# Kernel optimization log

Hardware: AMD Instinct MI355X
Metric: run time of the kernel (lower is better)

Reference implementation:

```python
import jax, jax.numpy as jnp
import numpy as np

H = 256  # rnn hidden size

def _rnn_dir(x, wih, whh, bih, bhh):
    # x: [B,T,D] -> outputs [B,T,H]; h_t = tanh(x_t Wih^T + bih + h_{t-1} Whh^T + bhh)
    xproj = jnp.einsum('btd,hd->bth', x, wih) + bih + bhh  # precompute input projection
    def step(h, xp):
        h = jnp.tanh(xp + h @ whh.T)
        return h, h
    h0 = jnp.zeros((x.shape[0], whh.shape[0]), x.dtype)
    _, ys = jax.lax.scan(step, h0, jnp.swapaxes(xproj, 0, 1))
    return jnp.swapaxes(ys, 0, 1)

def _birnn(x, wif, whf, bif, bhf, wib, whb, bib, bhb):
    fwd = _rnn_dir(x, wif, whf, bif, bhf)
    bwd = _rnn_dir(x[:, ::-1, :], wib, whb, bib, bhb)[:, ::-1, :]
    return jnp.concatenate([fwd, bwd], axis=-1)

def setup_inputs() -> dict:
    key = jax.random.key(0)
    ks = jax.random.split(key, 24)
    B, T, V, E = 64, 512, 131072, 128
    s = 0.05
    emb = jax.random.normal(ks[0], (V, E), jnp.float32) * s
    emb = emb.at[0].set(0.0)  # padding_idx=0
    def W(k, shp):
        return jax.random.normal(k, shp, jnp.float32) * s
    inp = {
        'x': jax.random.randint(ks[1], (B, T), 0, V),
        'emb': emb,
        'r1_wif': W(ks[2], (H, E)), 'r1_whf': W(ks[3], (H, H)),
        'r1_bif': W(ks[4], (H,)), 'r1_bhf': W(ks[5], (H,)),
        'r1_wib': W(ks[6], (H, E)), 'r1_whb': W(ks[7], (H, H)),
        'r1_bib': W(ks[8], (H,)), 'r1_bhb': W(ks[9], (H,)),
        'r2_wif': W(ks[10], (H, 2 * H)), 'r2_whf': W(ks[11], (H, H)),
        'r2_bif': W(ks[12], (H,)), 'r2_bhf': W(ks[13], (H,)),
        'r2_wib': W(ks[14], (H, 2 * H)), 'r2_whb': W(ks[15], (H, H)),
        'r2_bib': W(ks[16], (H,)), 'r2_bhb': W(ks[17], (H,)),
        'ln_g': jnp.ones((1024,), jnp.float32),
        'ln_b': jnp.zeros((1024,), jnp.float32),
        'w1': W(ks[18], (512, 1024)), 'b1': W(ks[19], (512,)),
        'w2': W(ks[20], (256, 512)), 'b2': W(ks[21], (256,)),
    }
    return inp

def reference(x, emb, r1_wif, r1_whf, r1_bif, r1_bhf, r1_wib, r1_whb, r1_bib, r1_bhb,
              r2_wif, r2_whf, r2_bif, r2_bhf, r2_wib, r2_whb, r2_bib, r2_bhb,
              ln_g, ln_b, w1, b1, w2, b2):
    e = emb[x]  # [B,T,128]
    o1 = _birnn(e, r1_wif, r1_whf, r1_bif, r1_bhf, r1_wib, r1_whb, r1_bib, r1_bhb)  # [B,T,512]
    o2 = _birnn(o1, r2_wif, r2_whf, r2_bif, r2_bhf, r2_wib, r2_whb, r2_bib, r2_bhb)  # [B,T,512]
    last = o2[:, -1, :]
    mean = jnp.mean(o2, axis=1)
    h = jnp.concatenate([last, mean], axis=1)  # [B,1024]
    mu = jnp.mean(h, axis=-1, keepdims=True)
    var = jnp.mean(jnp.square(h - mu), axis=-1, keepdims=True)
    h = (h - mu) * jax.lax.rsqrt(var + 1e-5) * ln_g + ln_b
    h = jax.nn.relu(h @ w1.T + b1)
    return h @ w2.T + b2
```

## Files before the change

kernel.cpp:

```cpp
#include <hip/hip_runtime.h>
#include <stdint.h>

typedef unsigned short u16;
typedef unsigned int   u32;
typedef __attribute__((ext_vector_type(8))) short short8;
typedef __attribute__((ext_vector_type(4))) float f32x4;

#define T_LEN 512
#define HID   256
#define C2LE 2.8853900817779268f

__device__ __forceinline__ float bflo(u32 u){ union{u32 i; float f;} v; v.i = u << 16; return v.f; }
__device__ __forceinline__ float bfhi(u32 u){ union{u32 i; float f;} v; v.i = u & 0xffff0000u; return v.f; }
__device__ __forceinline__ float b2f(u16 s){ union{u32 i; float f;} v; v.i = ((u32)s) << 16; return v.f; }
__device__ __forceinline__ u16 f2b(float f){
  union{float f; u32 i;} v; v.f = f;
  u32 r = v.i + 0x7fffu + ((v.i >> 16) & 1u);
  return (u16)(r >> 16);
}
__device__ __forceinline__ u32 pk2(float a, float b){ return (u32)f2b(a) | ((u32)f2b(b) << 16); }
__device__ __forceinline__ u32 cvtpk(float a, float b){
  u32 r; asm("v_cvt_pk_bf16_f32 %0, %1, %2" : "=v"(r) : "v"(a), "v"(b)); return r;
}
__device__ __forceinline__ float tanh_pre(float y){
#if __has_builtin(__builtin_amdgcn_exp2f)
  float e = __builtin_amdgcn_exp2f(y);
#else
  float e = exp2f(y);
#endif
  return __builtin_fmaf(-2.f, __builtin_amdgcn_rcpf(e + 1.f), 1.f);
}
__device__ __forceinline__ bool flag_bf16(const u32* f){ return (f[0] & 0xFFFFu) == 0x3F80u; }

#define NT 22
struct ConvArgs {
  const void* src[NT];
  u32 off[NT];
  u32 total;
  const u32* flagsrc;
};

__global__ __launch_bounds__(256)
void convert_params(ConvArgs a, u16* __restrict__ dst)
{
  const bool bf = flag_bf16(a.flagsrc);
  const u32 stride = gridDim.x * blockDim.x;
  for (u32 g = blockIdx.x * blockDim.x + threadIdx.x; g < a.total; g += stride) {
    int t = 0;
    #pragma unroll
    for (int i = 1; i < NT; ++i) t += (g >= a.off[i]);
    u32 local = g - a.off[t];
    float v = bf ? b2f(((const u16*)a.src[t])[local])
                 : ((const float*)a.src[t])[local];
    if (t == 1 || t == 5 || t == 9 || t == 13) v *= C2LE;
    dst[g] = f2b(v);
  }
}

template<int K, int SRC>
__global__ __launch_bounds__(256, 2)
void wgemm(const void* Bsrc, const int* __restrict__ gidx,
           const u16* __restrict__ Wf, const u16* __restrict__ Wb,
           const u16* __restrict__ bif, const u16* __restrict__ bhf,
           const u16* __restrict__ bib, const u16* __restrict__ bhb,
           u16* outT, const u32* flagsrc)
{
  __shared__ __align__(16) u16 lds[64 * K];
  const int tid  = threadIdx.x;
  const int row0 = blockIdx.x * 64;
  const int bb   = row0 >> 9;
  const int t0   = row0 & 511;
  const int bt   = bb >> 4, nb = bb & 15;
  constexpr int CPR = K / 8;

  bool abf = true;
  if (SRC == 0) abf = flag_bf16(flagsrc);

  for (int i = tid; i < 64 * CPR; i += 256) {
    int r = i / CPR, c = i % CPR;
    uint4 v;
    if (SRC == 0) {
      long rb = (long)gidx[row0 + r] * K;
      if (abf) {
        v = *(const uint4*)((const u16*)Bsrc + rb + c * 8);
      } else {
        const float* af = (const float*)Bsrc;
        float4 lo = *(const float4*)(af + rb + c * 8);
        float4 hi = *(const float4*)(af + rb + c * 8 + 4);
        v.x = pk2(lo.x, lo.y); v.y = pk2(lo.z, lo.w);
        v.z = pk2(hi.x, hi.y); v.w = pk2(hi.z, hi.w);
      }
    } else {
      int k = c * 8, d = k >> 8;
      size_t e = (size_t)(d * 4 + bt) * 2097152 + (size_t)(t0 + r) * 4096
               + (size_t)nb * 256 + (k & 255);
      v = *(const uint4*)((const u16*)Bsrc + e);
    }
    *(uint4*)&lds[r * K + ((c ^ (r & 7)) * 8)] = v;
  }
  __syncthreads();

  const int w = tid >> 6, lane = tid & 63, n16 = lane & 15, quad = lane >> 4;
  const int d = w >> 1;
  const u16* W  = d ? Wb : Wf;
  const u16* bi = d ? bib : bif;
  const u16* bh = d ? bhb : bhf;
  const int mbase = (w & 1) * 128;

  f32x4 acc[8][4];
  #pragma unroll
  for (int i = 0; i < 8; ++i)
    #pragma unroll
    for (int j = 0; j < 4; ++j) acc[i][j] = (f32x4){0.f, 0.f, 0.f, 0.f};

  #pragma unroll
  for (int kk = 0; kk < K / 32; ++kk) {
    short8 bfr[4];
    #pragma unroll
    for (int j = 0; j < 4; ++j) {
      int r = j * 16 + n16;
      int c = (kk * 4 + quad) ^ (r & 7);
      bfr[j] = *(const short8*)&lds[r * K + c * 8];
    }
    #pragma unroll
    for (int i = 0; i < 8; ++i) {
      short8 afr = *(const short8*)(W + (size_t)(mbase + i * 16 + n16) * K + kk * 32 + quad * 8);
      #pragma unroll
      for (int j = 0; j < 4; ++j)
        acc[i][j] = __builtin_amdgcn_mfma_f32_16x16x32_bf16(afr, bfr[j], acc[i][j], 0, 0, 0);
    }
  }

  #pragma unroll
  for (int i = 0; i < 8; ++i) {
    int mrow0 = mbase + i * 16 + quad * 4;
    uint2 biv = *(const uint2*)(bi + mrow0);
    uint2 bhv = *(const uint2*)(bh + mrow0);
    float bias0 = b2f(biv.x & 0xffff) + b2f(bhv.x & 0xffff);
    float bias1 = b2f(biv.x >> 16)    + b2f(bhv.x >> 16);
    float bias2 = b2f(biv.y & 0xffff) + b2f(bhv.y & 0xffff);
    float bias3 = b2f(biv.y >> 16)    + b2f(bhv.y >> 16);
    #pragma unroll
    for (int j = 0; j < 4; ++j) {
      int t = t0 + j * 16 + n16;
      uint2 pv;
      pv.x = cvtpk(C2LE * (acc[i][j][0] + bias0), C2LE * (acc[i][j][1] + bias1));
      pv.y = cvtpk(C2LE * (acc[i][j][2] + bias2), C2LE * (acc[i][j][3] + bias3));
      size_t e = (size_t)(d * 4 + bt) * 2097152 + (size_t)t * 4096
               + (size_t)nb * 256 + mrow0;
      *(uint2*)(outT + e) = pv;
    }
  }
}

template<int MODE>
__device__ __forceinline__ void scan_step5(
    int s, int send,
    const u16* hrp,
    u16* hwp,
    uint2& pf,
    const u16*& xptr, u16*& optr, int pstep,
    const short8 (&wa)[8], f32x4& sum, float* lastb, int lbase)
{
  short8 hb[8];
  #pragma unroll
  for (int kk = 0; kk < 8; ++kk)
    hb[kk] = *(const short8*)(hrp + kk * 32);

  uint2 xv = pf;
  pf = *(const uint2*)(xptr);
  xptr += pstep;

  f32x4 a = (f32x4){bflo(xv.x), bfhi(xv.x), bflo(xv.y), bfhi(xv.y)};
  f32x4 b = (f32x4){0.f, 0.f, 0.f, 0.f};
  #pragma unroll
  for (int kk = 0; kk < 8; kk += 2) {
    a = __builtin_amdgcn_mfma_f32_16x16x32_bf16(wa[kk],     hb[kk],     a, 0, 0, 0);
    b = __builtin_amdgcn_mfma_f32_16x16x32_bf16(wa[kk + 1], hb[kk + 1], b, 0, 0, 0);
  }

  float h0 = tanh_pre(a[0] + b[0]);
  float h1 = tanh_pre(a[1] + b[1]);
  float h2 = tanh_pre(a[2] + b[2]);
  float h3 = tanh_pre(a[3] + b[3]);
  uint2 hv; hv.x = cvtpk(h0, h1); hv.y = cvtpk(h2, h3);
  *(uint2*)(hwp) = hv;

  if (MODE == 0) {
    *(uint2*)(optr) = hv;
    optr += pstep;
  } else {
    sum += (f32x4){h0, h1, h2, h3};
    if (s == send)
      *(float4*)&lastb[lbase] = (float4){h0, h1, h2, h3};
  }

  asm volatile("s_waitcnt lgkmcnt(0)" ::: "memory");
  __builtin_amdgcn_s_barrier();
  asm volatile("" ::: "memory");
}

template<int MODE>
__global__ __launch_bounds__(1024, 4)
void rnn_scan(const u16* xpT,
              const u16* __restrict__ whhF, const u16* __restrict__ whhB,
              u16* o1T, float* __restrict__ lastb, float* __restrict__ sumb)
{
  __shared__ __align__(16) u16 hl[2][16][264];
  const int tid = threadIdx.x, w = tid >> 6, lane = tid & 63;
  const int n16 = lane & 15, quad = lane >> 4;
  const int dir = blockIdx.x >> 2, bt = blockIdx.x & 3;
  const u16* whh = dir ? whhB : whhF;
  const int m0 = w * 16 + quad * 4;

  short8 wa[8];
  #pragma unroll
  for (int kk = 0; kk < 8; ++kk)
    wa[kk] = *(const short8*)(whh + (size_t)(w * 16 + n16) * 256 + kk * 32 + quad * 8);

  for (int i = tid; i < 16 * 264; i += 1024) ((u16*)hl[0])[i] = 0;

  const size_t blkbase = (size_t)(dir * 4 + bt) * 2097152;
  const int t0    = dir ? 511 : 0;
  const int pstep = dir ? -4096 : 4096;
  const u16* xptr = xpT + blkbase + (size_t)t0 * 4096 + n16 * 256 + m0;
  u16*       optr = o1T + blkbase + (size_t)t0 * 4096 + n16 * 256 + m0;
  const int lbase = (dir * 64 + bt * 16 + n16) * 256 + m0;
  const int send  = dir ? 0 : 511;

  const u16* hr0 = &hl[0][n16][quad * 8];
  const u16* hr1 = &hl[1][n16][quad * 8];
  u16* hw0 = &hl[1][n16][m0];
  u16* hw1 = &hl[0][n16][m0];

  uint2 pf0, pf1;
  pf0 = *(const uint2*)(xptr); xptr += pstep;
  pf1 = *(const uint2*)(xptr); xptr += pstep;

  f32x4 sum = (f32x4){0.f, 0.f, 0.f, 0.f};
  __syncthreads();

  for (int s = 0; s < 512; s += 2) {
    scan_step5<MODE>(s,     send, hr0, hw0, pf0, xptr, optr, pstep, wa, sum, lastb, lbase);
    scan_step5<MODE>(s + 1, send, hr1, hw1, pf1, xptr, optr, pstep, wa, sum, lastb, lbase);
  }

  if (MODE == 1)
    *(float4*)&sumb[lbase] = (float4){sum[0], sum[1], sum[2], sum[3]};
}

__device__ __forceinline__ float dot8(uint4 q, const float* hp){
  return bflo(q.x)*hp[0] + bfhi(q.x)*hp[1] + bflo(q.y)*hp[2] + bfhi(q.y)*hp[3]
       + bflo(q.z)*hp[4] + bfhi(q.z)*hp[5] + bflo(q.w)*hp[6] + bfhi(q.w)*hp[7];
}

__global__ __launch_bounds__(256)
void head_kernel(const float* __restrict__ lastb, const float* __restrict__ sumb,
                 const u16* __restrict__ g, const u16* __restrict__ be,
                 const u16* __restrict__ w1, const u16* __restrict__ b1,
                 const u16* __restrict__ w2, const u16* __restrict__ b2,
                 void* outv, const u32* flagsrc)
{
  __shared__ __align__(16) float hv[1024];
  __shared__ __align__(16) float act[512];
  __shared__ float red[8];
  const int tid = threadIdx.x;
  const int b   = blockIdx.x;
  const bool bf = flag_bf16(flagsrc);

  float v0 = lastb[b * 256 + tid];
  float v1 = lastb[(64 + b) * 256 + tid];
  float v2 = sumb[b * 256 + tid] * (1.f / 512.f);
  float v3 = sumb[(64 + b) * 256 + tid] * (1.f / 512.f);
  hv[tid] = v0; hv[256 + tid] = v1; hv[512 + tid] = v2; hv[768 + tid] = v3;

  float s  = v0 + v1 + v2 + v3;
  float ss = v0*v0 + v1*v1 + v2*v2 + v3*v3;
  #pragma unroll
  for (int off = 32; off; off >>= 1) {
    s  += __shfl_down(s, off);
    ss += __shfl_down(ss, off);
  }
  if ((tid & 63) == 0) { red[tid >> 6] = s; red[4 + (tid >> 6)] = ss; }
  __syncthreads();
  float S  = red[0] + red[1] + red[2] + red[3];
  float SS = red[4] + red[5] + red[6] + red[7];
  float mu   = S * (1.f / 1024.f);
  float var  = SS * (1.f / 1024.f) - mu * mu;
  float rstd = rsqrtf(var + 1e-5f);

  #pragma unroll
  for (int i = 0; i < 4; ++i) {
    int idx = i * 256 + tid;
    hv[idx] = (hv[idx] - mu) * rstd * b2f(g[idx]) + b2f(be[idx]);
  }
  __syncthreads();

  #pragma unroll
  for (int jj = 0; jj < 2; ++jj) {
    int j = jj * 256 + tid;
    const uint4* wr = (const uint4*)(w1 + (long)j * 1024);
    float a = 0.f;
    for (int c = 0; c < 128; ++c) a += dot8(wr[c], &hv[c * 8]);
    a += b2f(b1[j]);
    act[j] = a > 0.f ? a : 0.f;
  }
  __syncthreads();

  const uint4* wr2 = (const uint4*)(w2 + (long)tid * 512);
  float a = 0.f;
  for (int c = 0; c < 64; ++c) a += dot8(wr2[c], &act[c * 8]);
  a += b2f(b2[tid]);

  if (bf) {
    ((u16*)outv)[b * 256 + tid] = f2b(a);
  } else {
    union { u32 i; float f; } u; u.i = ((u32)f2b(a)) << 16;
    ((float*)outv)[b * 256 + tid] = u.f;
  }
}

extern "C" void kernel_launch(void* const* d_in, const int* in_sizes, int n_in,
                              void* d_out, int out_size, void* d_ws, size_t ws_size,
                              hipStream_t stream)
{
  const int* x    = (const int*)d_in[0];
  const u32* flag = (const u32*)d_in[18];

  static const int sizes[NT] = {
    32768, 65536, 256, 256, 32768, 65536, 256, 256,
    131072, 65536, 256, 256, 131072, 65536, 256, 256,
    1024, 1024, 524288, 512, 131072, 256
  };
  ConvArgs ca;
  u32 off = 0;
  for (int i = 0; i < NT; ++i) {
    ca.src[i] = d_in[2 + i];
    ca.off[i] = off;
    off += (u32)sizes[i];
  }
  ca.total = off;
  ca.flagsrc = flag;

  char* ws = (char*)d_ws;
  u16*   buf    = (u16*)ws;
  u16*   pm     = (u16*)(ws + 33554432);
  float* lastb  = (float*)(ws + 36054528);
  float* sumb   = (float*)(ws + 36185600);

  const u16* p_r1wif = pm + 0;
  const u16* p_r1whf = pm + 32768;
  const u16* p_r1bif = pm + 98304;
  const u16* p_r1bhf = pm + 98560;
  const u16* p_r1wib = pm + 98816;
  const u16* p_r1whb = pm + 131584;
  const u16* p_r1bib = pm + 197120;
  const u16* p_r1bhb = pm + 197376;
  const u16* p_r2wif = pm + 197632;
  const u16* p_r2whf = pm + 328704;
  const u16* p_r2bif = pm + 394240;
  const u16* p_r2bhf = pm + 394496;
  const u16* p_r2wib = pm + 394752;
  const u16* p_r2whb = pm + 525824;
  const u16* p_r2bib = pm + 591360;
  const u16* p_r2bhb = pm + 591616;
  const u16* p_lng   = pm + 591872;
  const u16* p_lnb   = pm + 592896;
  const u16* p_w1    = pm + 593920;
  const u16* p_b1    = pm + 1118208;
  const u16* p_w2    = pm + 1118720;
  const u16* p_b2    = pm + 1249792;

  convert_params<<<1024, 256, 0, stream>>>(ca, pm);

  wgemm<128, 0><<<512, 256, 0, stream>>>(d_in[1], x,
      p_r1wif, p_r1wib, p_r1bif, p_r1bhf, p_r1bib, p_r1bhb, buf, flag);
  rnn_scan<0><<<8, 1024, 0, stream>>>(buf, p_r1whf, p_r1whb, buf, nullptr, nullptr);
  wgemm<512, 1><<<512, 256, 0, stream>>>(buf, nullptr,
      p_r2wif, p_r2wib, p_r2bif, p_r2bhf, p_r2bib, p_r2bhb, buf, flag);
  rnn_scan<1><<<8, 1024, 0, stream>>>(buf, p_r2whf, p_r2whb, nullptr, lastb, sumb);
  head_kernel<<<64, 256, 0, stream>>>(lastb, sumb, p_lng, p_lnb, p_w1, p_b1, p_w2, p_b2,
      d_out, flag);
}
```

Before: 948.6 us.

## Use 512-thread layer-2 scan with two 16-row output tiles per wave

Adds a new layer-2 RNN scan kernel that runs 8 waves per block instead of 16. Each wave computes two 16-row tiles of the hidden update, so the shared h fragments are reused across two weight tiles and fewer waves join each per-step barrier. The cost is twice the weight registers per wave and a longer MFMA chain per wave on every serial step. Layer 1 keeps the original 1024-thread scan.

```diff
diff --git a/kernel.cpp b/kernel.cpp
--- a/kernel.cpp
+++ b/kernel.cpp
@@ -156,9 +156,7 @@
 template<int MODE>
 __device__ __forceinline__ void scan_step5(
     int s, int send,
-    const u16* hrp,
-    u16* hwp,
-    uint2& pf,
+    const u16* hrp, u16* hwp, uint2& pf,
     const u16*& xptr, u16*& optr, int pstep,
     const short8 (&wa)[8], f32x4& sum, float* lastb, int lbase)
 {
@@ -247,6 +245,112 @@
 
   if (MODE == 1)
     *(float4*)&sumb[lbase] = (float4){sum[0], sum[1], sum[2], sum[3]};
+}
+
+__device__ __forceinline__ void scan_step8(
+    int s, int send,
+    const u16* hrp, u16* hwp, uint2 (&pf)[2],
+    const u16*& xptr, int pstep,
+    const short8 (&wa)[2][8], f32x4 (&sum)[2], float* lastb, int lbase)
+{
+  short8 hb[8];
+  #pragma unroll
+  for (int kk = 0; kk < 8; ++kk)
+    hb[kk] = *(const short8*)(hrp + kk * 32);
+
+  uint2 xv0 = pf[0], xv1 = pf[1];
+  pf[0] = *(const uint2*)(xptr);
+  pf[1] = *(const uint2*)(xptr + 16);
+  xptr += pstep;
+
+  f32x4 a0 = (f32x4){bflo(xv0.x), bfhi(xv0.x), bflo(xv0.y), bfhi(xv0.y)};
+  f32x4 a1 = (f32x4){bflo(xv1.x), bfhi(xv1.x), bflo(xv1.y), bfhi(xv1.y)};
+  f32x4 b0 = (f32x4){0.f, 0.f, 0.f, 0.f};
+  f32x4 b1 = (f32x4){0.f, 0.f, 0.f, 0.f};
+  #pragma unroll
+  for (int kk = 0; kk < 8; kk += 2) {
+    a0 = __builtin_amdgcn_mfma_f32_16x16x32_bf16(wa[0][kk],     hb[kk],     a0, 0, 0, 0);
+    a1 = __builtin_amdgcn_mfma_f32_16x16x32_bf16(wa[1][kk],     hb[kk],     a1, 0, 0, 0);
+    b0 = __builtin_amdgcn_mfma_f32_16x16x32_bf16(wa[0][kk + 1], hb[kk + 1], b0, 0, 0, 0);
+    b1 = __builtin_amdgcn_mfma_f32_16x16x32_bf16(wa[1][kk + 1], hb[kk + 1], b1, 0, 0, 0);
+  }
+
+  float h00 = tanh_pre(a0[0] + b0[0]), h01 = tanh_pre(a0[1] + b0[1]);
+  float h02 = tanh_pre(a0[2] + b0[2]), h03 = tanh_pre(a0[3] + b0[3]);
+  float h10 = tanh_pre(a1[0] + b1[0]), h11 = tanh_pre(a1[1] + b1[1]);
+  float h12 = tanh_pre(a1[2] + b1[2]), h13 = tanh_pre(a1[3] + b1[3]);
+
+  uint2 hv0; hv0.x = cvtpk(h00, h01); hv0.y = cvtpk(h02, h03);
+  uint2 hv1; hv1.x = cvtpk(h10, h11); hv1.y = cvtpk(h12, h13);
+  *(uint2*)(hwp)      = hv0;
+  *(uint2*)(hwp + 16) = hv1;
+
+  sum[0] += (f32x4){h00, h01, h02, h03};
+  sum[1] += (f32x4){h10, h11, h12, h13};
+  if (s == send) {
+    *(float4*)&lastb[lbase]      = (float4){h00, h01, h02, h03};
+    *(float4*)&lastb[lbase + 16] = (float4){h10, h11, h12, h13};
+  }
+
+  asm volatile("s_waitcnt lgkmcnt(0)" ::: "memory");
+  __builtin_amdgcn_s_barrier();
+  asm volatile("" ::: "memory");
+}
+
+__global__ __launch_bounds__(512, 2)
+void rnn_scan8(const u16* xpT,
+               const u16* __restrict__ whhF, const u16* __restrict__ whhB,
+               float* __restrict__ lastb, float* __restrict__ sumb)
+{
+  __shared__ __align__(16) u16 hl[2][16][264];
+  const int tid = threadIdx.x, w = tid >> 6, lane = tid & 63;
+  const int n16 = lane & 15, quad = lane >> 4;
+  const int dir = blockIdx.x >> 2, bt = blockIdx.x & 3;
+  const u16* whh = dir ? whhB : whhF;
+
+  short8 wa[2][8];
+  #pragma unroll
+  for (int j = 0; j < 2; ++j)
+    #pragma unroll
+    for (int kk = 0; kk < 8; ++kk)
+      wa[j][kk] = *(const short8*)(whh + (size_t)(w * 32 + j * 16 + n16) * 256
+                                       + kk * 32 + quad * 8);
+
+  for (int i = tid; i < 16 * 264; i += 512) ((u16*)hl[0])[i] = 0;
+
+  const size_t blkbase = (size_t)(dir * 4 + bt) * 2097152;
+  const int t0    = dir ? 511 : 0;
+  const int pstep = dir ? -4096 : 4096;
+  const int m0    = w * 32 + quad * 4;
+  const u16* xptr = xpT + blkbase + (size_t)t0 * 4096 + n16 * 256 + m0;
+  const int lbase = (dir * 64 + bt * 16 + n16) * 256 + m0;
+  const int send  = dir ? 0 : 511;
+
+  const u16* hr0 = &hl[0][n16][quad * 8];
+  const u16* hr1 = &hl[1][n16][quad * 8];
+  u16* hw0 = &hl[1][n16][m0];
+  u16* hw1 = &hl[0][n16][m0];
+
+  uint2 pf0[2], pf1[2];
+  pf0[0] = *(const uint2*)(xptr);
+  pf0[1] = *(const uint2*)(xptr + 16);
+  xptr += pstep;
+  pf1[0] = *(const uint2*)(xptr);
+  pf1[1] = *(const uint2*)(xptr + 16);
+  xptr += pstep;
+
+  f32x4 sum[2];
+  sum[0] = (f32x4){0.f, 0.f, 0.f, 0.f};
+  sum[1] = (f32x4){0.f, 0.f, 0.f, 0.f};
+  __syncthreads();
+
+  for (int s = 0; s < 512; s += 2) {
+    scan_step8(s,     send, hr0, hw0, pf0, xptr, pstep, wa, sum, lastb, lbase);
+    scan_step8(s + 1, send, hr1, hw1, pf1, xptr, pstep, wa, sum, lastb, lbase);
+  }
+
+  *(float4*)&sumb[lbase]      = (float4){sum[0][0], sum[0][1], sum[0][2], sum[0][3]};
+  *(float4*)&sumb[lbase + 16] = (float4){sum[1][0], sum[1][1], sum[1][2], sum[1][3]};
 }
 
 __device__ __forceinline__ float dot8(uint4 q, const float* hp){
@@ -378,7 +482,7 @@
   rnn_scan<0><<<8, 1024, 0, stream>>>(buf, p_r1whf, p_r1whb, buf, nullptr, nullptr);
   wgemm<512, 1><<<512, 256, 0, stream>>>(buf, nullptr,
       p_r2wif, p_r2wib, p_r2bif, p_r2bhf, p_r2bib, p_r2bhb, buf, flag);
-  rnn_scan<1><<<8, 1024, 0, stream>>>(buf, p_r2whf, p_r2whb, nullptr, lastb, sumb);
+  rnn_scan8<<<8, 512, 0, stream>>>(buf, p_r2whf, p_r2whb, lastb, sumb);
   head_kernel<<<64, 256, 0, stream>>>(lastb, sumb, p_lng, p_lnb, p_w1, p_b1, p_w2, p_b2,
       d_out, flag);
 }
```

Result: faster. 929.8 us (-2.0%).

## Split RNN scan batch rows across more workgroups with redundant MFMA columns

Applied to the files above, without the earlier changes.

The recurrent scan kernels now give each workgroup a subset of NB batch rows (8 for layer 1, 4 for layer 2) instead of 16, launching 16 or 32 workgroups instead of 8. The MFMA tile is still 16 columns wide, so lanes beyond NB compute duplicate columns and have their stores masked off. This spreads the serial per-timestep work over more compute units, cutting per-block latency and LDS pressure, at the cost of wasted MFMA throughput and repeated weight loads per block.

```diff
diff --git a/kernel.cpp b/kernel.cpp
--- a/kernel.cpp
+++ b/kernel.cpp
@@ -154,11 +154,9 @@
 }
 
 template<int MODE>
-__device__ __forceinline__ void scan_step5(
-    int s, int send,
-    const u16* hrp,
-    u16* hwp,
-    uint2& pf,
+__device__ __forceinline__ void scan_step6(
+    int s, int send, bool st,
+    const u16* hrp, u16* hwp, uint2& pf,
     const u16*& xptr, u16*& optr, int pstep,
     const short8 (&wa)[8], f32x4& sum, float* lastb, int lbase)
 {
@@ -184,14 +182,14 @@
   float h2 = tanh_pre(a[2] + b[2]);
   float h3 = tanh_pre(a[3] + b[3]);
   uint2 hv; hv.x = cvtpk(h0, h1); hv.y = cvtpk(h2, h3);
-  *(uint2*)(hwp) = hv;
+  if (st) *(uint2*)(hwp) = hv;
 
   if (MODE == 0) {
-    *(uint2*)(optr) = hv;
+    if (st) *(uint2*)(optr) = hv;
     optr += pstep;
   } else {
     sum += (f32x4){h0, h1, h2, h3};
-    if (s == send)
+    if (s == send && st)
       *(float4*)&lastb[lbase] = (float4){h0, h1, h2, h3};
   }
 
@@ -200,38 +198,45 @@
   asm volatile("" ::: "memory");
 }
 
-template<int MODE>
+template<int MODE, int NB>
 __global__ __launch_bounds__(1024, 4)
 void rnn_scan(const u16* xpT,
               const u16* __restrict__ whhF, const u16* __restrict__ whhB,
               u16* o1T, float* __restrict__ lastb, float* __restrict__ sumb)
 {
-  __shared__ __align__(16) u16 hl[2][16][264];
+  __shared__ __align__(16) u16 hl[2][NB][264];
   const int tid = threadIdx.x, w = tid >> 6, lane = tid & 63;
   const int n16 = lane & 15, quad = lane >> 4;
-  const int dir = blockIdx.x >> 2, bt = blockIdx.x & 3;
-  const u16* whh = dir ? whhB : whhF;
-  const int m0 = w * 16 + quad * 4;
+  constexpr int NSUB = 16 / NB;
+  constexpr int NBLK = 4 * NSUB;
+  const int dir   = blockIdx.x / NBLK;
+  const int rbl   = blockIdx.x % NBLK;
+  const int bt    = rbl / NSUB;
+  const int nbase = (rbl % NSUB) * NB;
+  const int rb    = n16 & (NB - 1);
+  const bool st   = (n16 < NB);
+  const u16* whh  = dir ? whhB : whhF;
+  const int m0    = w * 16 + quad * 4;
 
   short8 wa[8];
   #pragma unroll
   for (int kk = 0; kk < 8; ++kk)
     wa[kk] = *(const short8*)(whh + (size_t)(w * 16 + n16) * 256 + kk * 32 + quad * 8);
 
-  for (int i = tid; i < 16 * 264; i += 1024) ((u16*)hl[0])[i] = 0;
+  for (int i = tid; i < NB * 264; i += 1024) ((u16*)hl[0])[i] = 0;
 
   const size_t blkbase = (size_t)(dir * 4 + bt) * 2097152;
   const int t0    = dir ? 511 : 0;
   const int pstep = dir ? -4096 : 4096;
-  const u16* xptr = xpT + blkbase + (size_t)t0 * 4096 + n16 * 256 + m0;
-  u16*       optr = o1T + blkbase + (size_t)t0 * 4096 + n16 * 256 + m0;
-  const int lbase = (dir * 64 + bt * 16 + n16) * 256 + m0;
+  const u16* xptr = xpT + blkbase + (size_t)t0 * 4096 + (size_t)(nbase + rb) * 256 + m0;
+  u16*       optr = o1T + blkbase + (size_t)t0 * 4096 + (size_t)(nbase + rb) * 256 + m0;
+  const int lbase = (dir * 64 + bt * 16 + nbase + rb) * 256 + m0;
   const int send  = dir ? 0 : 511;
 
-  const u16* hr0 = &hl[0][n16][quad * 8];
-  const u16* hr1 = &hl[1][n16][quad * 8];
-  u16* hw0 = &hl[1][n16][m0];
-  u16* hw1 = &hl[0][n16][m0];
+  const u16* hr0 = &hl[0][rb][quad * 8];
+  const u16* hr1 = &hl[1][rb][quad * 8];
+  u16* hw0 = &hl[1][rb][m0];
+  u16* hw1 = &hl[0][rb][m0];
 
   uint2 pf0, pf1;
   pf0 = *(const uint2*)(xptr); xptr += pstep;
@@ -241,11 +246,11 @@
   __syncthreads();
 
   for (int s = 0; s < 512; s += 2) {
-    scan_step5<MODE>(s,     send, hr0, hw0, pf0, xptr, optr, pstep, wa, sum, lastb, lbase);
-    scan_step5<MODE>(s + 1, send, hr1, hw1, pf1, xptr, optr, pstep, wa, sum, lastb, lbase);
-  }
-
-  if (MODE == 1)
+    scan_step6<MODE>(s,     send, st, hr0, hw0, pf0, xptr, optr, pstep, wa, sum, lastb, lbase);
+    scan_step6<MODE>(s + 1, send, st, hr1, hw1, pf1, xptr, optr, pstep, wa, sum, lastb, lbase);
+  }
+
+  if (MODE == 1 && st)
     *(float4*)&sumb[lbase] = (float4){sum[0], sum[1], sum[2], sum[3]};
 }
 
@@ -375,10 +380,10 @@
 
   wgemm<128, 0><<<512, 256, 0, stream>>>(d_in[1], x,
       p_r1wif, p_r1wib, p_r1bif, p_r1bhf, p_r1bib, p_r1bhb, buf, flag);
-  rnn_scan<0><<<8, 1024, 0, stream>>>(buf, p_r1whf, p_r1whb, buf, nullptr, nullptr);
+  rnn_scan<0, 8><<<16, 1024, 0, stream>>>(buf, p_r1whf, p_r1whb, buf, nullptr, nullptr);
   wgemm<512, 1><<<512, 256, 0, stream>>>(buf, nullptr,
       p_r2wif, p_r2wib, p_r2bif, p_r2bhf, p_r2bib, p_r2bhb, buf, flag);
-  rnn_scan<1><<<8, 1024, 0, stream>>>(buf, p_r2whf, p_r2whb, nullptr, lastb, sumb);
+  rnn_scan<1, 4><<<32, 1024, 0, stream>>>(buf, p_r2whf, p_r2whb, nullptr, lastb, sumb);
   head_kernel<<<64, 256, 0, stream>>>(lastb, sumb, p_lng, p_lnb, p_w1, p_b1, p_w2, p_b2,
       d_out, flag);
 }
```

After: 912.9 us. 1.04x faster.
